# Kernel optimization log

Hardware: AMD Instinct MI355X
Metric: run time of the kernel (lower is better)

Reference implementation:

```python
import jax, jax.numpy as jnp
import numpy as np

B, L, V, DIN, H = 256, 256, 2048, 128, 256   # trees, leaves/tree, vocab, in_dim, mem_dim
NODES = 2 * L - 1                            # perfect binary tree, level-by-level layout
LEVELS = int(np.log2(L)) + 1                 # 9 levels: 256,128,...,1 nodes


def setup_inputs() -> dict:
    key = jax.random.key(0)
    ks = jax.random.split(key, 32)
    w = lambda k, shape: jax.random.normal(k, shape, jnp.float32) * 0.05
    inp = {
        "input_ids": jax.random.randint(ks[0], (B, NODES), 0, V),
        "emb": w(ks[1], (V, DIN)),
        # iou projections (i,o,u concatenated -> 3H)
        "Wioux": w(ks[2], (DIN, 3 * H)), "bioux": jnp.zeros((3 * H,), jnp.float32),
        "Wiouh1": w(ks[3], (H, 3 * H)), "biouh1": jnp.zeros((3 * H,), jnp.float32),
        "Wiouh2": w(ks[4], (H, 3 * H)), "biouh2": jnp.zeros((3 * H,), jnp.float32),
        # forget gates
        "Wfx": w(ks[5], (DIN, H)), "bfx": jnp.zeros((H,), jnp.float32),
        "Wfh11": w(ks[6], (H, H)), "bfh11": jnp.zeros((H,), jnp.float32),
        "Wfh12": w(ks[7], (H, H)), "bfh12": jnp.zeros((H,), jnp.float32),
        "Wfh21": w(ks[8], (H, H)), "bfh21": jnp.zeros((H,), jnp.float32),
        "Wfh22": w(ks[9], (H, H)), "bfh22": jnp.zeros((H,), jnp.float32),
        # classifier head
        "Wl1": w(ks[10], (H, 100)), "bl1": jnp.zeros((100,), jnp.float32),
        "Wl2": w(ks[11], (100, 1)), "bl2": jnp.zeros((1,), jnp.float32),
    }
    return inp


def reference(input_ids, emb, Wioux, bioux, Wiouh1, biouh1, Wiouh2, biouh2,
              Wfx, bfx, Wfh11, bfh11, Wfh12, bfh12, Wfh21, bfh21, Wfh22, bfh22,
              Wl1, bl1, Wl2, bl2):
    emb = emb.at[0].set(0.0)                 # padding_idx=0
    xemb = emb[input_ids]                    # [B, NODES, DIN]

    def cell(x, h1, h2, c1, c2):
        iou = (x @ Wioux + bioux) + (h1 @ Wiouh1 + biouh1) + (h2 @ Wiouh2 + biouh2)
        i, o, u = jnp.split(iou, 3, axis=-1)
        i, o, u = jax.nn.sigmoid(i), jax.nn.sigmoid(o), jnp.tanh(u)
        fx = x @ Wfx + bfx
        f0 = jax.nn.sigmoid((h1 @ Wfh11 + bfh11) + (h2 @ Wfh12 + bfh12) + fx)
        f1 = jax.nn.sigmoid((h1 @ Wfh21 + bfh21) + (h2 @ Wfh22 + bfh22) + fx)
        c = i * u + f0 * c1 + f1 * c2
        h = o * jnp.tanh(c)
        return h, c

    # leaves: zero child states
    z = jnp.zeros((B, L, H), jnp.float32)
    h, c = cell(xemb[:, :L], z, z, z, z)     # [B, L, H]

    off, n = 0, L
    for _ in range(LEVELS - 1):              # fixed small structural loop (8 iters)
        off += n
        n //= 2
        x = xemb[:, off:off + n]             # [B, n, DIN]
        h, c = cell(x, h[:, 0::2], h[:, 1::2], c[:, 0::2], c[:, 1::2])

    root_h = h[:, 0]                         # [B, H]
    hid = root_h @ Wl1 + bl1                 # linear1
    pred = (jax.nn.relu(hid) @ Wl2 + bl2)[..., 0]   # [B], arithmetic head (no softmax)
    return pred
```

## Files before the change

kernel.cpp:

```cpp
#include <hip/hip_runtime.h>
#include <math.h>

#define B_ 256
#define L_ 256
#define V_ 2048
#define DIN_ 128
#define H_ 256
#define NODES_ 511

typedef _Float16 half8 __attribute__((ext_vector_type(8)));
typedef float f32x4 __attribute__((ext_vector_type(4)));

__device__ __forceinline__ float sigm(float x) { return 1.f / (1.f + __expf(-x)); }
__device__ __forceinline__ float tanh_f(float x) {
    float xc = fminf(fmaxf(x, -15.f), 15.f);
    float e = __expf(2.f * xc);
    return (e - 1.f) / (e + 1.f);
}
__device__ __forceinline__ void gload16(const void* g, void* l) {
    __builtin_amdgcn_global_load_lds((const __attribute__((address_space(1))) unsigned int*)g,
                                     (__attribute__((address_space(3))) unsigned int*)l, 16, 0, 0);
}
template<int N> __device__ __forceinline__ void vwaitN() {
    asm volatile("s_waitcnt vmcnt(%0)" :: "i"(N) : "memory");
}

__global__ void build_WT(_Float16* __restrict__ WT,
    const float* __restrict__ Wioux, const float* __restrict__ Wfx,
    const float* __restrict__ Wiouh1, const float* __restrict__ Wfh11, const float* __restrict__ Wfh21,
    const float* __restrict__ Wiouh2, const float* __restrict__ Wfh12, const float* __restrict__ Wfh22)
{
    int e = blockIdx.x * 256 + threadIdx.x;
    int nn = e / 640, k = e - nn * 640;
    int g = nn >> 8, t = nn & 255;
    float v;
    if (k < 128) {
        v = (g < 3) ? Wioux[k * 768 + nn] : Wfx[k * 256 + t];
    } else if (k < 384) {
        int kp = k - 128;
        v = (g < 3) ? Wiouh1[kp * 768 + nn] : ((g == 3) ? Wfh11[kp * 256 + t] : Wfh21[kp * 256 + t]);
    } else {
        int kp = k - 384;
        v = (g < 3) ? Wiouh2[kp * 768 + nn] : ((g == 3) ? Wfh12[kp * 256 + t] : Wfh22[kp * 256 + t]);
    }
    WT[e] = (_Float16)v;
}

__global__ void build_bias(float* __restrict__ bias,
    const float* __restrict__ bioux, const float* __restrict__ biouh1, const float* __restrict__ biouh2,
    const float* __restrict__ bfx, const float* __restrict__ bfh11, const float* __restrict__ bfh12,
    const float* __restrict__ bfh21, const float* __restrict__ bfh22)
{
    int e = blockIdx.x * 256 + threadIdx.x;
    if (e >= 1280) return;
    int g = e >> 8, t = e & 255;
    float v;
    if (g < 3)       v = bioux[e] + biouh1[e] + biouh2[e];
    else if (g == 3) v = bfx[t] + bfh11[t] + bfh12[t];
    else             v = bfx[t] + bfh21[t] + bfh22[t];
    bias[e] = v;
}

__global__ void build_embh(_Float16* __restrict__ EH, const float* __restrict__ emb) {
    int e = blockIdx.x * 256 + threadIdx.x;
    EH[e] = (e < DIN_) ? (_Float16)0.f : (_Float16)emb[e];
}

__global__ __launch_bounds__(256) void build_table(float* __restrict__ tab, const float* __restrict__ emb,
    const float* __restrict__ Wioux, const float* __restrict__ Wfx,
    const float* __restrict__ bioux, const float* __restrict__ biouh1, const float* __restrict__ biouh2,
    const float* __restrict__ bfx, const float* __restrict__ bfh11, const float* __restrict__ bfh12,
    const float* __restrict__ bfh21, const float* __restrict__ bfh22)
{
    __shared__ float As[64][33];
    __shared__ float Ws[32][65];
    const int tid = threadIdx.x, tx = tid & 15, ty = tid >> 4;
    const int i0 = blockIdx.x * 64, c0 = blockIdx.y * 64;
    const int g = c0 >> 8;
    float acc[4][4];
    #pragma unroll
    for (int i = 0; i < 4; ++i)
        #pragma unroll
        for (int j = 0; j < 4; ++j) acc[i][j] = 0.f;

    for (int k0 = 0; k0 < 128; k0 += 32) {
        #pragma unroll
        for (int it = 0; it < 2; ++it) {
            int f = tid + it * 256;
            int row = f >> 3, kk = (f & 7) * 4;
            int gr = i0 + row;
            float4 av = (gr == 0) ? make_float4(0.f, 0.f, 0.f, 0.f)
                                  : *(const float4*)(emb + (size_t)gr * 128 + k0 + kk);
            As[row][kk] = av.x; As[row][kk + 1] = av.y; As[row][kk + 2] = av.z; As[row][kk + 3] = av.w;
            int k = f >> 4, cc = (f & 15) * 4;
            int col = c0 + cc;
            float4 wv = (g < 3) ? *(const float4*)(Wioux + (size_t)(k0 + k) * 768 + col)
                                : *(const float4*)(Wfx + (size_t)(k0 + k) * 256 + (col & 255));
            Ws[k][cc] = wv.x; Ws[k][cc + 1] = wv.y; Ws[k][cc + 2] = wv.z; Ws[k][cc + 3] = wv.w;
        }
        __syncthreads();
        #pragma unroll 8
        for (int k = 0; k < 32; ++k) {
            float a[4], w[4];
            #pragma unroll
            for (int i = 0; i < 4; ++i) a[i] = As[ty * 4 + i][k];
            #pragma unroll
            for (int j = 0; j < 4; ++j) w[j] = Ws[k][tx * 4 + j];
            #pragma unroll
            for (int i = 0; i < 4; ++i)
                #pragma unroll
                for (int j = 0; j < 4; ++j) acc[i][j] = fmaf(a[i], w[j], acc[i][j]);
        }
        __syncthreads();
    }
    #pragma unroll
    for (int j = 0; j < 4; ++j) {
        int col = c0 + tx * 4 + j; int t = col & 255;
        float bs = (g < 3) ? (bioux[col] + biouh1[col] + biouh2[col])
                 : (g == 3) ? (bfx[t] + bfh11[t] + bfh12[t])
                            : (bfx[t] + bfh21[t] + bfh22[t]);
        #pragma unroll
        for (int i = 0; i < 4; ++i)
            tab[(size_t)(i0 + ty * 4 + i) * 1280 + col] = acc[i][j] + bs;
    }
}

__global__ void build_h0c0(const float* __restrict__ tab, _Float16* __restrict__ H0h, float* __restrict__ H0c) {
    int id = blockIdx.x, t = threadIdx.x;
    const float* tp = tab + (size_t)id * 1280 + t;
    float vi = sigm(tp[0]), vo = sigm(tp[256]), vu = tanh_f(tp[512]);
    float c = vi * vu;
    H0h[id * 256 + t] = (_Float16)(vo * tanh_f(c));
    H0c[id * 256 + t] = c;
}

template<bool LVL1, int RT>
__global__ __launch_bounds__(256, (RT >= 4 ? 2 : 4)) void cellJ(
    const _Float16* __restrict__ WT, const float* __restrict__ bias,
    const _Float16* __restrict__ embh, const int* __restrict__ ids,
    const _Float16* __restrict__ h_prev, const float* __restrict__ c_prev,
    _Float16* __restrict__ h_out, float* __restrict__ c_out,
    int n, int ln, int off, int nx)
{
    constexpr int BM = RT * 64;
    __shared__ __align__(16) char Asm[3][BM * 64];
    __shared__ __align__(16) char Bsm[3][5120];
    const int tid = threadIdx.x, lane = tid & 63, wid = tid >> 6;
    const int l15 = lane & 15, lg = lane >> 4;

    int bid = blockIdx.x, x, y;
    if ((nx & 7) == 0) { int xcd = bid & 7, rank = bid >> 3; x = xcd * (nx >> 3) + (rank >> 4); y = rank & 15; }
    else { x = bid >> 4; y = bid & 15; }
    const int rowB = x * BM;
    const int t0 = y * 16;

    const unsigned segOff = (unsigned)((((lane & 3) ^ ((lane >> 3) & 3))) * 16);
    unsigned srcX[RT], srcA[RT], srcB1_[LVL1 ? RT : 1];
    #pragma unroll
    for (int i = 0; i < RT; ++i) {
        int rl = (wid * RT + i) * 16 + (lane >> 2);
        int r = rowB + rl;
        int b = r >> ln, j = r & (n - 1);
        srcX[i] = (unsigned)ids[b * NODES_ + off + j] * 256u + segOff;
        if constexpr (LVL1) {
            int bb = r >> 7, jj = r & 127;
            srcA[i]   = (unsigned)ids[bb * NODES_ + 2 * jj] * 512u + segOff;
            srcB1_[i] = (unsigned)ids[bb * NODES_ + 2 * jj + 1] * 512u + segOff;
        } else {
            srcA[i] = (unsigned)r * 1024u + segOff;
        }
    }
    unsigned bsrc0, bsrc1 = 0;
    {
        int nr = tid >> 2, j = tid & 3;
        int ng = (nr >> 4) * 256 + t0 + (nr & 15);
        bsrc0 = (unsigned)((ng * 640 + ((j ^ ((nr >> 1) & 3)) * 8)) * 2);
        if (wid == 0) {
            int ng2 = 1024 + t0 + (tid >> 2);
            int seg2 = (tid & 3) ^ ((tid >> 3) & 3);
            bsrc1 = (unsigned)((ng2 * 640 + seg2 * 8) * 2);
        }
    }
    const char* hPB = (const char*)h_prev;
    const char* xPB = (const char*)embh;
    const char* wPB = (const char*)WT;

    f32x4 acc[RT][5];
    #pragma unroll
    for (int rt = 0; rt < RT; ++rt)
        #pragma unroll
        for (int g = 0; g < 5; ++g) acc[rt][g] = (f32x4)0.f;

    const int xw = (l15 >> 1) & 3;

    auto STAGE = [&](int st, int buf) {
        #pragma unroll
        for (int i = 0; i < RT; ++i) {
            const char* bp; unsigned sa;
            if (st < 4) { bp = xPB; sa = srcX[i] + (unsigned)st * 64u; }
            else if constexpr (LVL1) {
                bp = hPB;
                sa = (st < 12) ? (srcA[i] + (unsigned)(st - 4) * 64u)
                               : (srcB1_[i] + (unsigned)(st - 12) * 64u);
            } else { bp = hPB; sa = srcA[i] + (unsigned)(st - 4) * 64u; }
            gload16(bp + sa, &Asm[buf][(wid * RT + i) * 1024 + lane * 16]);
        }
        gload16(wPB + bsrc0 + (unsigned)st * 64u, &Bsm[buf][tid * 16]);
        if (wid == 0) gload16(wPB + bsrc1 + (unsigned)st * 64u, &Bsm[buf][4096 + tid * 16]);
    };
    auto COMPUTE = [&](int buf) {
        half8 aF[RT];
        #pragma unroll
        for (int rt = 0; rt < RT; ++rt)
            aF[rt] = *(const half8*)&Asm[buf][(wid * RT * 16 + rt * 16 + l15) * 64 + ((lg ^ xw) * 16)];
        #pragma unroll
        for (int g = 0; g < 5; ++g) {
            half8 bF = *(const half8*)&Bsm[buf][(g * 16 + l15) * 64 + ((lg ^ xw) * 16)];
            #pragma unroll
            for (int rt = 0; rt < RT; ++rt)
                acc[rt][g] = __builtin_amdgcn_mfma_f32_16x16x32_f16(aF[rt], bF, acc[rt][g], 0, 0, 0);
        }
    };
    auto WAITB = [&](bool counted) {
        if (counted) { if (wid == 0) vwaitN<RT + 2>(); else vwaitN<RT + 1>(); }
        else vwaitN<0>();
        __builtin_amdgcn_s_barrier();
        __builtin_amdgcn_sched_barrier(0);
    };

    STAGE(0, 0);
    STAGE(1, 1);
    WAITB(true);

    #pragma unroll
    for (int S = 0; S < 20; ++S) {
        if (S + 2 < 20) STAGE(S + 2, (S + 2) % 3);
        COMPUTE(S % 3);
        if (S < 19) WAITB(S + 2 < 20);
    }

    const int tcol = t0 + l15;
    const float b0 = bias[tcol], b1 = bias[256 + tcol], b2 = bias[512 + tcol];
    const float b3 = bias[768 + tcol], b4 = bias[1024 + tcol];
    #pragma unroll
    for (int rt = 0; rt < RT; ++rt) {
        #pragma unroll
        for (int q = 0; q < 4; ++q) {
            int row = rowB + wid * (RT * 16) + rt * 16 + lg * 4 + q;
            float c1, c2;
            if constexpr (LVL1) {
                int bb = row >> 7, jj = row & 127;
                c1 = c_prev[(size_t)ids[bb * NODES_ + 2 * jj] * 256 + tcol];
                c2 = c_prev[(size_t)ids[bb * NODES_ + 2 * jj + 1] * 256 + tcol];
            } else {
                const float* cpp = c_prev + (size_t)row * 512 + tcol;
                c1 = cpp[0]; c2 = cpp[256];
            }
            float vi  = sigm(acc[rt][0][q] + b0);
            float vo  = sigm(acc[rt][1][q] + b1);
            float vu  = tanh_f(acc[rt][2][q] + b2);
            float vf0 = sigm(acc[rt][3][q] + b3);
            float vf1 = sigm(acc[rt][4][q] + b4);
            float c = vi * vu + vf0 * c1 + vf1 * c2;
            size_t ob = (size_t)row * 256 + tcol;
            h_out[ob] = (_Float16)(vo * tanh_f(c));
            c_out[ob] = c;
        }
    }
}

__global__ void head_kernel(const _Float16* __restrict__ hroot,
    const float* __restrict__ Wl1, const float* __restrict__ bl1,
    const float* __restrict__ Wl2, const float* __restrict__ bl2,
    float* __restrict__ out)
{
    __shared__ float hrow[H_];
    __shared__ float red[256];
    int b = blockIdx.x; int tid = threadIdx.x;
    hrow[tid] = (float)hroot[(size_t)b * H_ + tid];
    __syncthreads();
    float v = 0.f;
    if (tid < 100) {
        float s = bl1[tid];
        for (int k = 0; k < H_; ++k) s = fmaf(hrow[k], Wl1[k * 100 + tid], s);
        v = fmaxf(s, 0.f) * Wl2[tid];
    }
    red[tid] = v;
    __syncthreads();
    for (int s = 128; s > 0; s >>= 1) { if (tid < s) red[tid] += red[tid + s]; __syncthreads(); }
    if (tid == 0) out[b] = red[0] + bl2[0];
}

extern "C" void kernel_launch(void* const* d_in, const int* in_sizes, int n_in,
                              void* d_out, int out_size, void* d_ws, size_t ws_size,
                              hipStream_t stream) {
    const int*   ids    = (const int*)d_in[0];
    const float* emb    = (const float*)d_in[1];
    const float* Wioux  = (const float*)d_in[2];
    const float* bioux  = (const float*)d_in[3];
    const float* Wiouh1 = (const float*)d_in[4];
    const float* biouh1 = (const float*)d_in[5];
    const float* Wiouh2 = (const float*)d_in[6];
    const float* biouh2 = (const float*)d_in[7];
    const float* Wfx    = (const float*)d_in[8];
    const float* bfx    = (const float*)d_in[9];
    const float* Wfh11  = (const float*)d_in[10];
    const float* bfh11  = (const float*)d_in[11];
    const float* Wfh12  = (const float*)d_in[12];
    const float* bfh12  = (const float*)d_in[13];
    const float* Wfh21  = (const float*)d_in[14];
    const float* bfh21  = (const float*)d_in[15];
    const float* Wfh22  = (const float*)d_in[16];
    const float* bfh22  = (const float*)d_in[17];
    const float* Wl1    = (const float*)d_in[18];
    const float* bl1    = (const float*)d_in[19];
    const float* Wl2    = (const float*)d_in[20];
    const float* bl2    = (const float*)d_in[21];
    float* out = (float*)d_out;

    char* wsb = (char*)d_ws;
    _Float16* WT   = (_Float16*)(wsb);
    _Float16* embh = (_Float16*)(wsb + 1638400);
    float*    bias = (float*)(wsb + 2162688);
    float*    tab  = (float*)(wsb + 2167808);
    _Float16* H0h  = (_Float16*)(wsb + 12653568);
    float*    H0c  = (float*)(wsb + 13702144);
    _Float16* hA   = (_Float16*)(wsb + 15799296);
    _Float16* hB   = (_Float16*)(wsb + 24187904);
    float*    cA   = (float*)(wsb + 40965120);
    float*    cB   = (float*)(wsb + 57742336);

    build_WT<<<dim3(3200), 256, 0, stream>>>(WT, Wioux, Wfx, Wiouh1, Wfh11, Wfh21, Wiouh2, Wfh12, Wfh22);
    build_bias<<<dim3(5), 256, 0, stream>>>(bias, bioux, biouh1, biouh2, bfx, bfh11, bfh12, bfh21, bfh22);
    build_embh<<<dim3(1024), 256, 0, stream>>>(embh, emb);
    build_table<<<dim3(32, 20), 256, 0, stream>>>(tab, emb, Wioux, Wfx,
        bioux, biouh1, biouh2, bfx, bfh11, bfh12, bfh21, bfh22);
    build_h0c0<<<dim3(2048), 256, 0, stream>>>(tab, H0h, H0c);

    cellJ<true, 4><<<dim3(2048), 256, 0, stream>>>(WT, bias, embh, ids, H0h, H0c, hB, cB, 128, 7, 256, 128);

    _Float16 *hp = hB, *hn = hA;
    float    *cp = cB, *cn = cA;
    int off = 384, n = 64, ln = 6;
    for (int lvl = 2; lvl <= 8; ++lvl) {
        int M = B_ * n;
        if (M >= 2048) {
            int nx = M / 256;
            cellJ<false, 4><<<dim3(nx * 16), 256, 0, stream>>>(WT, bias, embh, ids, hp, cp, hn, cn, n, ln, off, nx);
        } else if (M >= 1024) {
            int nx = M / 128;
            cellJ<false, 2><<<dim3(nx * 16), 256, 0, stream>>>(WT, bias, embh, ids, hp, cp, hn, cn, n, ln, off, nx);
        } else {
            int nx = M / 64;
            cellJ<false, 1><<<dim3(nx * 16), 256, 0, stream>>>(WT, bias, embh, ids, hp, cp, hn, cn, n, ln, off, nx);
        }
        off += n; n >>= 1; --ln;
        _Float16* t1 = hp; hp = hn; hn = t1;
        float*    t2 = cp; cp = cn; cn = t2;
    }

    head_kernel<<<dim3(256), 256, 0, stream>>>(hp, Wl1, bl1, Wl2, bl2, out);
}
```

Before: 278.2 us.

## Precompute per-vocab child recurrent projections for level-1 and gather-combine

Since level-1 children are leaves whose h/c depend only on token id, compute a per-vocab table G of their recurrent projections with a small GEMM. Level 1 is then a gather of the x-table and two G rows plus gate math, replacing the full per-node GEMM. This trades a large per-node matmul for a 2048-row GEMM and gather-heavy memory traffic over a ~21MB buffer. The LVL1 path in cellJ is simplified accordingly.

```diff
diff --git a/kernel.cpp b/kernel.cpp
--- a/kernel.cpp
+++ b/kernel.cpp
@@ -134,6 +134,120 @@
     H0c[id * 256 + t] = c;
 }
 
+__global__ __launch_bounds__(256, 2) void build_G(
+    const _Float16* __restrict__ WT, const _Float16* __restrict__ H0h, float* __restrict__ G)
+{
+    __shared__ __align__(16) char Asm[3][256 * 64];
+    __shared__ __align__(16) char Bsm[3][4096];
+    const int tid = threadIdx.x, lane = tid & 63, wid = tid >> 6;
+    const int l15 = lane & 15, lg = lane >> 4;
+    const int rowB = blockIdx.x * 256;
+    const int C0 = blockIdx.y * 64;
+
+    const unsigned segOff = (unsigned)((((lane & 3) ^ ((lane >> 3) & 3))) * 16);
+    unsigned srcA[4];
+    #pragma unroll
+    for (int i = 0; i < 4; ++i) {
+        int rl = (wid * 4 + i) * 16 + (lane >> 2);
+        srcA[i] = (unsigned)(rowB + rl) * 512u + segOff;
+    }
+    unsigned bsrc;
+    {
+        int cc = tid >> 2, j = tid & 3;
+        int np = C0 + cc;
+        int part = (np >= 1280) ? 1 : 0;
+        int nn = np - part * 1280;
+        bsrc = (unsigned)((nn * 640 + 128 + part * 256 + ((j ^ ((cc >> 1) & 3)) * 8)) * 2);
+    }
+    const char* hPB = (const char*)H0h;
+    const char* wPB = (const char*)WT;
+
+    f32x4 acc[4][4];
+    #pragma unroll
+    for (int rt = 0; rt < 4; ++rt)
+        #pragma unroll
+        for (int ct = 0; ct < 4; ++ct) acc[rt][ct] = (f32x4)0.f;
+
+    const int xw = (l15 >> 1) & 3;
+
+    auto STAGE = [&](int st, int buf) {
+        #pragma unroll
+        for (int i = 0; i < 4; ++i)
+            gload16(hPB + srcA[i] + (unsigned)st * 64u, &Asm[buf][(wid * 4 + i) * 1024 + lane * 16]);
+        gload16(wPB + bsrc + (unsigned)st * 64u, &Bsm[buf][tid * 16]);
+    };
+    auto COMPUTE = [&](int buf) {
+        half8 aF[4];
+        #pragma unroll
+        for (int rt = 0; rt < 4; ++rt)
+            aF[rt] = *(const half8*)&Asm[buf][(wid * 64 + rt * 16 + l15) * 64 + ((lg ^ xw) * 16)];
+        #pragma unroll
+        for (int ct = 0; ct < 4; ++ct) {
+            int cc = ct * 16 + l15;
+            half8 bF = *(const half8*)&Bsm[buf][cc * 64 + ((lg ^ ((cc >> 1) & 3)) * 16)];
+            #pragma unroll
+            for (int rt = 0; rt < 4; ++rt)
+                acc[rt][ct] = __builtin_amdgcn_mfma_f32_16x16x32_f16(aF[rt], bF, acc[rt][ct], 0, 0, 0);
+        }
+    };
+    auto WAITB = [&](bool counted) {
+        if (counted) vwaitN<5>(); else vwaitN<0>();
+        __builtin_amdgcn_s_barrier();
+        __builtin_amdgcn_sched_barrier(0);
+    };
+
+    STAGE(0, 0); STAGE(1, 1); WAITB(true);
+    #pragma unroll
+    for (int S = 0; S < 8; ++S) {
+        if (S + 2 < 8) STAGE(S + 2, (S + 2) % 3);
+        COMPUTE(S % 3);
+        if (S < 7) WAITB(S + 2 < 8);
+    }
+
+    #pragma unroll
+    for (int rt = 0; rt < 4; ++rt)
+        #pragma unroll
+        for (int ct = 0; ct < 4; ++ct)
+            #pragma unroll
+            for (int q = 0; q < 4; ++q)
+                G[(size_t)(rowB + wid * 64 + rt * 16 + lg * 4 + q) * 2560 + C0 + ct * 16 + l15] = acc[rt][ct][q];
+}
+
+__global__ __launch_bounds__(256) void lvl1_combine(
+    const float* __restrict__ tab, const float* __restrict__ G,
+    const float* __restrict__ H0c, const int* __restrict__ ids,
+    _Float16* __restrict__ h_out, float* __restrict__ c_out)
+{
+    const int tid = threadIdx.x;
+    const int l15 = tid & 15, rq = tid >> 4;
+    const int bid = blockIdx.x;
+    const int p = bid & 15, rb = bid >> 4;
+    const int col = p * 16 + l15;
+    #pragma unroll 4
+    for (int it = 0; it < 16; ++it) {
+        int row = rb * 256 + it * 16 + rq;
+        int b = row >> 7, j = row & 127;
+        const int* idr = ids + b * NODES_;
+        int idp = idr[256 + j];
+        int idA = idr[2 * j];
+        int idB = idr[2 * j + 1];
+        const float* tp = tab + (size_t)idp * 1280 + col;
+        const float* g1 = G + (size_t)idA * 2560 + col;
+        const float* g2 = G + (size_t)idB * 2560 + 1280 + col;
+        float pre0 = tp[0]    + g1[0]    + g2[0];
+        float pre1 = tp[256]  + g1[256]  + g2[256];
+        float pre2 = tp[512]  + g1[512]  + g2[512];
+        float pre3 = tp[768]  + g1[768]  + g2[768];
+        float pre4 = tp[1024] + g1[1024] + g2[1024];
+        float c1 = H0c[idA * 256 + col], c2 = H0c[idB * 256 + col];
+        float vi = sigm(pre0), vo = sigm(pre1), vu = tanh_f(pre2);
+        float vf0 = sigm(pre3), vf1 = sigm(pre4);
+        float c = vi * vu + vf0 * c1 + vf1 * c2;
+        h_out[(size_t)row * 256 + col] = (_Float16)(vo * tanh_f(c));
+        c_out[(size_t)row * 256 + col] = c;
+    }
+}
+
 template<bool LVL1, int RT>
 __global__ __launch_bounds__(256, (RT >= 4 ? 2 : 4)) void cellJ(
     const _Float16* __restrict__ WT, const float* __restrict__ bias,
@@ -155,20 +269,14 @@
     const int t0 = y * 16;
 
     const unsigned segOff = (unsigned)((((lane & 3) ^ ((lane >> 3) & 3))) * 16);
-    unsigned srcX[RT], srcA[RT], srcB1_[LVL1 ? RT : 1];
+    unsigned srcX[RT], srcA[RT];
     #pragma unroll
     for (int i = 0; i < RT; ++i) {
         int rl = (wid * RT + i) * 16 + (lane >> 2);
         int r = rowB + rl;
         int b = r >> ln, j = r & (n - 1);
         srcX[i] = (unsigned)ids[b * NODES_ + off + j] * 256u + segOff;
-        if constexpr (LVL1) {
-            int bb = r >> 7, jj = r & 127;
-            srcA[i]   = (unsigned)ids[bb * NODES_ + 2 * jj] * 512u + segOff;
-            srcB1_[i] = (unsigned)ids[bb * NODES_ + 2 * jj + 1] * 512u + segOff;
-        } else {
-            srcA[i] = (unsigned)r * 1024u + segOff;
-        }
+        srcA[i] = (unsigned)r * 1024u + segOff;
     }
     unsigned bsrc0, bsrc1 = 0;
     {
@@ -198,11 +306,7 @@
         for (int i = 0; i < RT; ++i) {
             const char* bp; unsigned sa;
             if (st < 4) { bp = xPB; sa = srcX[i] + (unsigned)st * 64u; }
-            else if constexpr (LVL1) {
-                bp = hPB;
-                sa = (st < 12) ? (srcA[i] + (unsigned)(st - 4) * 64u)
-                               : (srcB1_[i] + (unsigned)(st - 12) * 64u);
-            } else { bp = hPB; sa = srcA[i] + (unsigned)(st - 4) * 64u; }
+            else { bp = hPB; sa = srcA[i] + (unsigned)(st - 4) * 64u; }
             gload16(bp + sa, &Asm[buf][(wid * RT + i) * 1024 + lane * 16]);
         }
         gload16(wPB + bsrc0 + (unsigned)st * 64u, &Bsm[buf][tid * 16]);
@@ -247,15 +351,8 @@
         #pragma unroll
         for (int q = 0; q < 4; ++q) {
             int row = rowB + wid * (RT * 16) + rt * 16 + lg * 4 + q;
-            float c1, c2;
-            if constexpr (LVL1) {
-                int bb = row >> 7, jj = row & 127;
-                c1 = c_prev[(size_t)ids[bb * NODES_ + 2 * jj] * 256 + tcol];
-                c2 = c_prev[(size_t)ids[bb * NODES_ + 2 * jj + 1] * 256 + tcol];
-            } else {
-                const float* cpp = c_prev + (size_t)row * 512 + tcol;
-                c1 = cpp[0]; c2 = cpp[256];
-            }
+            const float* cpp = c_prev + (size_t)row * 512 + tcol;
+            float c1 = cpp[0], c2 = cpp[256];
             float vi  = sigm(acc[rt][0][q] + b0);
             float vo  = sigm(acc[rt][1][q] + b1);
             float vu  = tanh_f(acc[rt][2][q] + b2);
@@ -329,6 +426,7 @@
     _Float16* hB   = (_Float16*)(wsb + 24187904);
     float*    cA   = (float*)(wsb + 40965120);
     float*    cB   = (float*)(wsb + 57742336);
+    float*    G    = (float*)(wsb + 91296768);
 
     build_WT<<<dim3(3200), 256, 0, stream>>>(WT, Wioux, Wfx, Wiouh1, Wfh11, Wfh21, Wiouh2, Wfh12, Wfh22);
     build_bias<<<dim3(5), 256, 0, stream>>>(bias, bioux, biouh1, biouh2, bfx, bfh11, bfh12, bfh21, bfh22);
@@ -336,8 +434,9 @@
     build_table<<<dim3(32, 20), 256, 0, stream>>>(tab, emb, Wioux, Wfx,
         bioux, biouh1, biouh2, bfx, bfh11, bfh12, bfh21, bfh22);
     build_h0c0<<<dim3(2048), 256, 0, stream>>>(tab, H0h, H0c);
-
-    cellJ<true, 4><<<dim3(2048), 256, 0, stream>>>(WT, bias, embh, ids, H0h, H0c, hB, cB, 128, 7, 256, 128);
+    build_G<<<dim3(8, 40), 256, 0, stream>>>(WT, H0h, G);
+
+    lvl1_combine<<<dim3(2048), 256, 0, stream>>>(tab, G, H0c, ids, hB, cB);
 
     _Float16 *hp = hB, *hn = hA;
     float    *cp = cB, *cn = cA;
```

After: 311.9 us. +12.1%, slower.
